# Performance work log

Measured on AMD Instinct MI355X. Metric: run time of the kernel, lower is better.

Reference implementation:

```python
import jax, jax.numpy as jnp
import numpy as np

N_EMBD = 1024
N_HEADS = 16
HEAD_DIM = N_EMBD // N_HEADS


def setup_inputs() -> dict:
    key = jax.random.key(0)
    ks = jax.random.split(key, 6)
    s = 1.0 / np.sqrt(N_EMBD)
    x = jax.random.normal(ks[0], (2, 2048, N_EMBD), dtype=jnp.float32)
    # torch Linear weights are [out, in]; y = x @ W.T
    Wk = jax.random.uniform(ks[1], (N_EMBD, N_EMBD), jnp.float32, -s, s)
    Wq = jax.random.uniform(ks[2], (N_EMBD, N_EMBD), jnp.float32, -s, s)
    Wv = jax.random.uniform(ks[3], (N_EMBD, N_EMBD), jnp.float32, -s, s)
    Wp = jax.random.uniform(ks[4], (N_EMBD, N_EMBD), jnp.float32, -s, s)
    bp = jax.random.uniform(ks[5], (N_EMBD,), jnp.float32, -s, s)
    return {"x": x, "Wq": Wq, "Wk": Wk, "Wv": Wv, "Wp": Wp, "bp": bp}


def reference(x, Wq, Wk, Wv, Wp, bp):
    B, T, C = x.shape
    H, D = N_HEADS, HEAD_DIM
    # projections (torch Linear: x @ W.T), reshape to [B, H, T, D]
    q = (x @ Wq.T).reshape(B, T, H, D).transpose(0, 2, 1, 3)
    k = (x @ Wk.T).reshape(B, T, H, D).transpose(0, 2, 1, 3)
    v = (x @ Wv.T).reshape(B, T, H, D).transpose(0, 2, 1, 3)
    # scaled causal attention, full [B,H,T,T] scores (faithful to original)
    att = jnp.einsum('bhqd,bhkd->bhqk', q, k) * (D ** -0.5)
    causal = jnp.tril(jnp.ones((T, T), dtype=bool))
    att = jnp.where(causal[None, None], att, -jnp.inf)
    att = jax.nn.softmax(att, axis=-1)
    out = jnp.einsum('bhqk,bhkd->bhqd', att, v)
    out = out.transpose(0, 2, 1, 3).reshape(B, T, C)
    return out @ Wp.T + bp
```

## Files before the change

kernel.cpp:

```cpp
#include <hip/hip_runtime.h>

typedef __bf16 bf16;
typedef __bf16 bf16x8 __attribute__((ext_vector_type(8)));
typedef float f32x4 __attribute__((ext_vector_type(4)));

typedef __attribute__((address_space(1))) const void as1_void;
typedef __attribute__((address_space(3))) void as3_void;

#define DEV __device__ __forceinline__
#define NEG_BIG (-1.0e30f)


DEV void async_load16(const void* g, void* l) {
  __builtin_amdgcn_global_load_lds((as1_void*)g, (as3_void*)l, 16, 0, 0);
}
DEV bf16x8 load8(const bf16* p) { bf16x8 v; __builtin_memcpy(&v, p, 16); return v; }
DEV void store8(bf16* p, bf16x8 v) { __builtin_memcpy(p, &v, 16); }

DEV int sniff_bf16(const unsigned short* __restrict__ xr) {
  const int lane = threadIdx.x & 63;
  const unsigned short w = xr[lane * 2];
  const int e = (w >> 7) & 0xFF;
  const bool sane = ((w & 0x7FFF) == 0) || (e >= 97 && e <= 157);
  return __popcll(__ballot(sane)) >= 48;
}

struct ConvArgs {
  const void* src[6];
  bf16* dst[6];
  int n[6];
};

__global__ __launch_bounds__(256) void convert_kernel(ConvArgs a) {
  const int isbf = sniff_bf16((const unsigned short*)a.src[0]);
  const int t = blockIdx.y;
  const int n = a.n[t];
  bf16* d = a.dst[t];
  const int stride = gridDim.x * 256 * 8;
  if (isbf) {
    const bf16* s = (const bf16*)a.src[t];
    for (int i = (blockIdx.x * 256 + threadIdx.x) * 8; i < n; i += stride)
      store8(d + i, load8(s + i));
  } else {
    const float* s = (const float*)a.src[t];
    for (int i = (blockIdx.x * 256 + threadIdx.x) * 8; i < n; i += stride) {
      float tmp[8];
      __builtin_memcpy(tmp, s + i, 32);
      bf16x8 v;
#pragma unroll
      for (int j = 0; j < 8; ++j) v[j] = (bf16)tmp[j];
      store8(d + i, v);
    }
  }
}

DEV void gemm_core_128(const bf16* A, const bf16* W, int K, int m0, int n0,
                       f32x4 (&acc)[4][4]) {
  __shared__ alignas(16) bf16 As[2][128 * 64];
  __shared__ alignas(16) bf16 Bs[2][128 * 64];
  const int tid = threadIdx.x;
  const int lane = tid & 63;
  const int wid = tid >> 6;
  const int wm = (wid >> 1) << 6;
  const int wn = (wid & 1) << 6;
  const int lr = lane & 15;
  const int lg = lane >> 4;

  const f32x4 zero = {0.f, 0.f, 0.f, 0.f};
#pragma unroll
  for (int i = 0; i < 4; ++i)
#pragma unroll
    for (int j = 0; j < 4; ++j) acc[i][j] = zero;

  const int nt = K >> 6;

  auto stage = [&](int buf, int t) {
    const int k0 = t << 6;
#pragma unroll
    for (int it = 0; it < 4; ++it) {
      const int lin = it * 256 + tid;
      const int row = lin >> 3;
      const int sc = (lin & 7) ^ (row & 7);
      async_load16(A + (size_t)(m0 + row) * K + (size_t)(k0 + sc * 8),
                   &As[buf][0] + lin * 8);
      async_load16(W + (size_t)(n0 + row) * K + (size_t)(k0 + sc * 8),
                   &Bs[buf][0] + lin * 8);
    }
  };

  auto compute = [&](int buf) {
    const bf16* as = &As[buf][0];
    const bf16* bs = &Bs[buf][0];
#pragma unroll
    for (int kk = 0; kk < 64; kk += 32) {
      const int g0 = kk >> 3;
      bf16x8 af[4], bfr[4];
#pragma unroll
      for (int i = 0; i < 4; ++i) {
        const int r = wm + i * 16 + lr;
        af[i] = load8(as + ((r << 3) | ((g0 + lg) ^ (r & 7))) * 8);
      }
#pragma unroll
      for (int j = 0; j < 4; ++j) {
        const int r = wn + j * 16 + lr;
        bfr[j] = load8(bs + ((r << 3) | ((g0 + lg) ^ (r & 7))) * 8);
      }
#pragma unroll
      for (int i = 0; i < 4; ++i)
#pragma unroll
        for (int j = 0; j < 4; ++j)
          acc[i][j] = __builtin_amdgcn_mfma_f32_16x16x32_bf16(af[i], bfr[j], acc[i][j], 0, 0, 0);
    }
  };

  stage(0, 0);
  stage(1, 1);
  int cur = 0;
  for (int t = 0; t < nt; ++t) {
    if (t + 1 < nt) asm volatile("s_waitcnt vmcnt(8)" ::: "memory");
    else            asm volatile("s_waitcnt vmcnt(0)" ::: "memory");
    __builtin_amdgcn_s_barrier();
    compute(cur);
    asm volatile("s_waitcnt lgkmcnt(0)" ::: "memory");
    __builtin_amdgcn_s_barrier();
    if (t + 2 < nt) stage(cur, t + 2);
    cur ^= 1;
  }
}

DEV size_t frag_idx(int row, int col) {
  return ((size_t)(((col >> 5) * 4 + ((row >> 4) & 3)) * 64 + ((col >> 3) & 3) * 16 + (row & 15)) << 3)
         | (size_t)(col & 7);
}

__global__ __launch_bounds__(256) void qkv_proj_kernel(
    const bf16* __restrict__ x, const bf16* __restrict__ Wq,
    const bf16* __restrict__ Wk, const bf16* __restrict__ Wv,
    bf16* __restrict__ q_ws, bf16* __restrict__ k_ws, bf16* __restrict__ vt_ws) {
  const int L = blockIdx.x;
  const int xcd = L & 7;
  const int i2 = L >> 3;
  const int m0 = (xcd * 4 + (i2 & 3)) << 7;
  const int rest = i2 >> 2;
  const int n0 = (rest & 7) << 7;
  const int mode = rest >> 3;
  const bf16* W = (mode == 0) ? Wq : (mode == 1) ? Wk : Wv;
  f32x4 acc[4][4];
  gemm_core_128(x, W, 1024, m0, n0, acc);

  const int tid = threadIdx.x;
  const int lane = tid & 63, wid = tid >> 6;
  const int wm = (wid >> 1) << 6, wn = (wid & 1) << 6;
  const int lr = lane & 15, lg = lane >> 4;
  bf16* out = (mode == 0) ? q_ws : (mode == 1) ? k_ws : vt_ws;
#pragma unroll
  for (int i = 0; i < 4; ++i) {
#pragma unroll
    for (int r = 0; r < 4; ++r) {
      const int m = m0 + wm + i * 16 + lg * 4 + r;
      const int b = m >> 11, t = m & 2047;
#pragma unroll
      for (int j = 0; j < 4; ++j) {
        const int n = n0 + wn + j * 16 + lr;
        const int h = n >> 6, d = n & 63;
        const float v = acc[i][j][r];
        const size_t base = ((size_t)(b * 16 + h) << 17) + ((size_t)(t >> 6) << 12);
        const size_t idx = base + ((mode < 2) ? frag_idx(t & 63, d) : frag_idx(d, t & 63));
        out[idx] = (bf16)v;
      }
    }
  }
}

__global__ __launch_bounds__(256, 2) void attn_kernel(
    const bf16* __restrict__ q_ws, const bf16* __restrict__ k_ws,
    const bf16* __restrict__ vt_ws, bf16* __restrict__ a_ws) {
  const int L = blockIdx.x;
  const int xcd = L & 7;
  const int bh = xcd * 4 + ((L >> 3) & 3);
  const int pr = L >> 5;
  const int tid = threadIdx.x;
  const int lane = tid & 63, w = tid >> 6;
  const int lr = lane & 15, lg = lane >> 4;
  const int fo = lg * 16 + lr;

  __shared__ alignas(16) bf16 Ps[4][16 * 72];
  bf16* ps = &Ps[w][0];

  const size_t hb = (size_t)bh << 17;
  const int b = bh >> 4, h = bh & 15;
  const f32x4 zero = {0.f, 0.f, 0.f, 0.f};

  for (int ph = 0; ph < 2; ++ph) {
    const int qt = ph ? (31 - pr) : pr;
    const size_t qtb = hb + ((size_t)qt << 12);

    bf16x8 aq[2];
#pragma unroll
    for (int c2 = 0; c2 < 2; ++c2)
      aq[c2] = load8(q_ws + qtb + (size_t)(((c2 * 4 + w) * 64 + fo) << 3));

    f32x4 o_acc[4];
#pragma unroll
    for (int j = 0; j < 4; ++j) o_acc[j] = zero;
    float lsum[4] = {0.f, 0.f, 0.f, 0.f};

    auto load_k = [&](bf16x8 (&bk)[4][2], int kt) {
      const size_t ktb = hb + ((size_t)kt << 12);
#pragma unroll
      for (int j = 0; j < 4; ++j)
#pragma unroll
        for (int c2 = 0; c2 < 2; ++c2)
          bk[j][c2] = load8(k_ws + ktb + (size_t)(((c2 * 4 + j) * 64 + fo) << 3));
    };

    auto step = [&](const bf16x8 (&bk)[4][2], int kt, bool diag) {
      const size_t ktb = hb + ((size_t)kt << 12);
      bf16x8 bv[4][2];
#pragma unroll
      for (int j = 0; j < 4; ++j)
#pragma unroll
        for (int c2 = 0; c2 < 2; ++c2)
          bv[j][c2] = load8(vt_ws + ktb + (size_t)(((c2 * 4 + j) * 64 + fo) << 3));

      f32x4 s[4];
#pragma unroll
      for (int j = 0; j < 4; ++j) {
        s[j] = __builtin_amdgcn_mfma_f32_16x16x32_bf16(aq[0], bk[j][0], zero, 0, 0, 0);
        s[j] = __builtin_amdgcn_mfma_f32_16x16x32_bf16(aq[1], bk[j][1], s[j], 0, 0, 0);
      }
      float p[4][4];
#pragma unroll
      for (int j = 0; j < 4; ++j) {
#pragma unroll
        for (int r = 0; r < 4; ++r) {
          float v = s[j][r] * 0.125f;
          if (diag && (j * 16 + lr) > (w * 16 + lg * 4 + r)) v = NEG_BIG;
          p[j][r] = __expf(v);
        }
      }
#pragma unroll
      for (int r = 0; r < 4; ++r)
        lsum[r] += (p[0][r] + p[1][r]) + (p[2][r] + p[3][r]);
#pragma unroll
      for (int j = 0; j < 4; ++j)
#pragma unroll
        for (int r = 0; r < 4; ++r)
          ps[(lg * 4 + r) * 72 + j * 16 + lr] = (bf16)p[j][r];
#pragma unroll
      for (int c2 = 0; c2 < 2; ++c2) {
        const bf16x8 ap = load8(ps + lr * 72 + c2 * 32 + lg * 8);
#pragma unroll
        for (int j = 0; j < 4; ++j)
          o_acc[j] = __builtin_amdgcn_mfma_f32_16x16x32_bf16(ap, bv[j][c2], o_acc[j], 0, 0, 0);
      }
    };

    bf16x8 bkA[4][2], bkB[4][2];
    const int n = qt;
    load_k(bkA, qt);
    if (n > 0) load_k(bkB, 0);
    step(bkA, qt, true);
    int kt = 0;
    while (kt + 1 < n) {
      load_k(bkA, kt + 1);
      step(bkB, kt, false);
      if (kt + 2 < n) load_k(bkB, kt + 2);
      step(bkA, kt + 1, false);
      kt += 2;
    }
    if (kt < n) step(bkB, kt, false);

    float l_i[4];
#pragma unroll
    for (int r = 0; r < 4; ++r) {
      float v = lsum[r];
#pragma unroll
      for (int off = 1; off < 16; off <<= 1) v += __shfl_xor(v, off, 64);
      l_i[r] = v;
    }

#pragma unroll
    for (int r = 0; r < 4; ++r) {
      const int t = qt * 64 + w * 16 + lg * 4 + r;
      const float inv = 1.f / l_i[r];
#pragma unroll
      for (int j = 0; j < 4; ++j) {
        const size_t idx = (((size_t)(b * 2048 + t)) << 10) | (size_t)(h * 64 + j * 16 + lr);
        a_ws[idx] = (bf16)(o_acc[j][r] * inv);
      }
    }
  }
}

__global__ __launch_bounds__(256) void out_proj_kernel(
    const bf16* __restrict__ A, const bf16* __restrict__ Wp,
    const bf16* __restrict__ bp, void* __restrict__ out,
    const unsigned short* __restrict__ xraw) {
  const int L = blockIdx.x;
  const int xcd = L & 7;
  const int i2 = L >> 3;
  const int m0 = (xcd * 4 + (i2 & 3)) << 7;
  const int n0 = (i2 >> 2) << 7;
  f32x4 acc[4][4];
  gemm_core_128(A, Wp, 1024, m0, n0, acc);

  const int tid = threadIdx.x;
  const int lane = tid & 63, wid = tid >> 6;
  const int wm = (wid >> 1) << 6, wn = (wid & 1) << 6;
  const int lr = lane & 15, lg = lane >> 4;
  const int isbf = sniff_bf16(xraw);
#pragma unroll
  for (int i = 0; i < 4; ++i) {
#pragma unroll
    for (int r = 0; r < 4; ++r) {
      const int m = m0 + wm + i * 16 + lg * 4 + r;
#pragma unroll
      for (int j = 0; j < 4; ++j) {
        const int n = n0 + wn + j * 16 + lr;
        const float v = acc[i][j][r] + (float)bp[n];
        const size_t idx = ((size_t)m << 10) | (size_t)n;
        if (isbf) ((bf16*)out)[idx] = (bf16)v;
        else      ((float*)out)[idx] = v;
      }
    }
  }
}

extern "C" void kernel_launch(void* const* d_in, const int* in_sizes, int n_in,
                              void* d_out, int out_size, void* d_ws, size_t ws_size,
                              hipStream_t stream) {
  (void)in_sizes; (void)n_in; (void)out_size;
  if (ws_size < (50u << 20)) return;

  char* ws = (char*)d_ws;
  bf16* q_ws  = (bf16*)(ws);
  bf16* k_ws  = (bf16*)(ws + (8u << 20));
  bf16* vt_ws = (bf16*)(ws + (16u << 20));
  bf16* a_ws  = (bf16*)(ws + (24u << 20));
  bf16* xc    = (bf16*)(ws + (32u << 20));
  bf16* Wqc   = (bf16*)(ws + (40u << 20));
  bf16* Wkc   = (bf16*)(ws + (42u << 20));
  bf16* Wvc   = (bf16*)(ws + (44u << 20));
  bf16* Wpc   = (bf16*)(ws + (46u << 20));
  bf16* bpc   = (bf16*)(ws + (48u << 20));

  ConvArgs ca;
  ca.src[0] = d_in[0]; ca.dst[0] = xc;  ca.n[0] = 4096 * 1024;
  ca.src[1] = d_in[1]; ca.dst[1] = Wqc; ca.n[1] = 1024 * 1024;
  ca.src[2] = d_in[2]; ca.dst[2] = Wkc; ca.n[2] = 1024 * 1024;
  ca.src[3] = d_in[3]; ca.dst[3] = Wvc; ca.n[3] = 1024 * 1024;
  ca.src[4] = d_in[4]; ca.dst[4] = Wpc; ca.n[4] = 1024 * 1024;
  ca.src[5] = d_in[5]; ca.dst[5] = bpc; ca.n[5] = 1024;
  convert_kernel<<<dim3(512, 6), 256, 0, stream>>>(ca);

  qkv_proj_kernel<<<768, 256, 0, stream>>>(xc, Wqc, Wkc, Wvc, q_ws, k_ws, vt_ws);
  attn_kernel<<<512, 256, 0, stream>>>(q_ws, k_ws, vt_ws, a_ws);
  out_proj_kernel<<<256, 256, 0, stream>>>(a_ws, Wpc, bpc, d_out,
                                           (const unsigned short*)d_in[0]);
}
```

Measured before the change: 182.2 us.

## Use triple-buffered K=32 pipelined GEMM core for QKV projection

Adds a GEMM core that stages 128x32 tiles of A and W into three LDS buffers via async global-to-LDS loads with an XOR swizzle, issuing loads two steps ahead and waiting with a single barrier per K step. The QKV projection kernel now uses it instead of the double-buffered K=64 core. The aim is to hide global load latency and cut barrier stalls, at the cost of more loop iterations and smaller compute per stage.

Result: faster. 178.3 us (-2.1%).

```diff
diff --git a/kernel.cpp b/kernel.cpp
--- a/kernel.cpp
+++ b/kernel.cpp
@@ -54,6 +54,92 @@
   }
 }
 
+DEV void gemm_core_128_p(const bf16* A, const bf16* W, const int K, int m0, int n0,
+                         f32x4 (&acc)[4][4]) {
+  __shared__ alignas(16) bf16 As[3][128 * 32];
+  __shared__ alignas(16) bf16 Bs[3][128 * 32];
+  const int tid = threadIdx.x;
+  const int lane = tid & 63;
+  const int wid = tid >> 6;
+  const int wm = (wid >> 1) << 6;
+  const int wn = (wid & 1) << 6;
+  const int lr = lane & 15;
+  const int lg = lane >> 4;
+
+  size_t srcA[2], srcB[2];
+  int ldsoff[2];
+#pragma unroll
+  for (int it = 0; it < 2; ++it) {
+    const int lin = it * 256 + tid;
+    const int lr2 = lin >> 3, c = lin & 7;
+    const int u = c ^ (lr2 & 7);
+    const int r = lr2 * 2 + (u >> 2);
+    const int g = u & 3;
+    srcA[it] = (size_t)(m0 + r) * K + (size_t)(g * 8);
+    srcB[it] = (size_t)(n0 + r) * K + (size_t)(g * 8);
+    ldsoff[it] = lin * 8;
+  }
+  int offA[4], offB[4];
+#pragma unroll
+  for (int i = 0; i < 4; ++i) {
+    const int r = wm + i * 16 + lr;
+    const int cc = (lg | ((r & 1) << 2)) ^ ((r >> 1) & 7);
+    offA[i] = (((r >> 1) << 3) | cc) * 8;
+  }
+#pragma unroll
+  for (int j = 0; j < 4; ++j) {
+    const int r = wn + j * 16 + lr;
+    const int cc = (lg | ((r & 1) << 2)) ^ ((r >> 1) & 7);
+    offB[j] = (((r >> 1) << 3) | cc) * 8;
+  }
+
+  const f32x4 zero = {0.f, 0.f, 0.f, 0.f};
+#pragma unroll
+  for (int i = 0; i < 4; ++i)
+#pragma unroll
+    for (int j = 0; j < 4; ++j) acc[i][j] = zero;
+
+  const int nt = K >> 5;
+
+  auto stage = [&](int buf, int t) {
+    const size_t k0 = (size_t)(t << 5);
+#pragma unroll
+    for (int it = 0; it < 2; ++it) {
+      async_load16(A + srcA[it] + k0, &As[buf][0] + ldsoff[it]);
+      async_load16(W + srcB[it] + k0, &Bs[buf][0] + ldsoff[it]);
+    }
+  };
+
+  auto compute = [&](int buf) {
+    const bf16* as = &As[buf][0];
+    const bf16* bs = &Bs[buf][0];
+    bf16x8 af[4], bfr[4];
+#pragma unroll
+    for (int i = 0; i < 4; ++i) af[i] = load8(as + offA[i]);
+#pragma unroll
+    for (int j = 0; j < 4; ++j) bfr[j] = load8(bs + offB[j]);
+    __builtin_amdgcn_s_setprio(1);
+#pragma unroll
+    for (int i = 0; i < 4; ++i)
+#pragma unroll
+      for (int j = 0; j < 4; ++j)
+        acc[i][j] = __builtin_amdgcn_mfma_f32_16x16x32_bf16(af[i], bfr[j], acc[i][j], 0, 0, 0);
+    __builtin_amdgcn_s_setprio(0);
+  };
+
+  stage(0, 0);
+  stage(1, 1);
+  int b0 = 0, b1 = 1, b2 = 2;
+  for (int t = 0; t < nt; ++t) {
+    if (t + 1 < nt) asm volatile("s_waitcnt vmcnt(4)" ::: "memory");
+    else            asm volatile("s_waitcnt vmcnt(0)" ::: "memory");
+    __builtin_amdgcn_s_barrier();
+    if (t + 2 < nt) stage(b2, t + 2);
+    compute(b0);
+    const int tmp = b0; b0 = b1; b1 = b2; b2 = tmp;
+  }
+}
+
 DEV void gemm_core_128(const bf16* A, const bf16* W, int K, int m0, int n0,
                        f32x4 (&acc)[4][4]) {
   __shared__ alignas(16) bf16 As[2][128 * 64];
@@ -146,7 +232,7 @@
   const int mode = rest >> 3;
   const bf16* W = (mode == 0) ? Wq : (mode == 1) ? Wk : Wv;
   f32x4 acc[4][4];
-  gemm_core_128(x, W, 1024, m0, n0, acc);
+  gemm_core_128_p(x, W, 1024, m0, n0, acc);
 
   const int tid = threadIdx.x;
   const int lane = tid & 63, wid = tid >> 6;
```

## Triple-buffer GEMM with K=32 tiles and one-tile-per-block attention grid

Applied to the files above, without the earlier changes.

The shared GEMM core moves from double-buffered 64-wide K tiles to triple-buffered 32-wide K tiles. Source and LDS offsets are precomputed once, one barrier per iteration is removed by issuing the next stage before compute, and MFMA issue priority is raised with setprio. The attention kernel now gives each block a single query tile, heaviest first, on a 1024-block grid instead of pairing light and heavy tiles in 512 blocks. This trades explicit load balancing for more parallelism and dynamic scheduling, and the GEMM uses smaller tiles with deeper prefetch.

New measurement: 183.5 us. No clear change (+0.8%).

```diff
diff --git a/kernel.cpp b/kernel.cpp
--- a/kernel.cpp
+++ b/kernel.cpp
@@ -54,10 +54,10 @@
   }
 }
 
-DEV void gemm_core_128(const bf16* A, const bf16* W, int K, int m0, int n0,
-                       f32x4 (&acc)[4][4]) {
-  __shared__ alignas(16) bf16 As[2][128 * 64];
-  __shared__ alignas(16) bf16 Bs[2][128 * 64];
+DEV void gemm_core_128_p(const bf16* A, const bf16* W, const int K, int m0, int n0,
+                         f32x4 (&acc)[4][4]) {
+  __shared__ alignas(16) bf16 As[3][128 * 32];
+  __shared__ alignas(16) bf16 Bs[3][128 * 32];
   const int tid = threadIdx.x;
   const int lane = tid & 63;
   const int wid = tid >> 6;
@@ -66,65 +66,77 @@
   const int lr = lane & 15;
   const int lg = lane >> 4;
 
+  size_t srcA[2], srcB[2];
+  int ldsoff[2];
+#pragma unroll
+  for (int it = 0; it < 2; ++it) {
+    const int lin = it * 256 + tid;
+    const int lr2 = lin >> 3, c = lin & 7;
+    const int u = c ^ (lr2 & 7);
+    const int r = lr2 * 2 + (u >> 2);
+    const int g = u & 3;
+    srcA[it] = (size_t)(m0 + r) * K + (size_t)(g * 8);
+    srcB[it] = (size_t)(n0 + r) * K + (size_t)(g * 8);
+    ldsoff[it] = lin * 8;
+  }
+  int offA[4], offB[4];
+#pragma unroll
+  for (int i = 0; i < 4; ++i) {
+    const int r = wm + i * 16 + lr;
+    const int cc = (lg | ((r & 1) << 2)) ^ ((r >> 1) & 7);
+    offA[i] = (((r >> 1) << 3) | cc) * 8;
+  }
+#pragma unroll
+  for (int j = 0; j < 4; ++j) {
+    const int r = wn + j * 16 + lr;
+    const int cc = (lg | ((r & 1) << 2)) ^ ((r >> 1) & 7);
+    offB[j] = (((r >> 1) << 3) | cc) * 8;
+  }
+
   const f32x4 zero = {0.f, 0.f, 0.f, 0.f};
 #pragma unroll
   for (int i = 0; i < 4; ++i)
 #pragma unroll
     for (int j = 0; j < 4; ++j) acc[i][j] = zero;
 
-  const int nt = K >> 6;
+  const int nt = K >> 5;
 
   auto stage = [&](int buf, int t) {
-    const int k0 = t << 6;
-#pragma unroll
-    for (int it = 0; it < 4; ++it) {
-      const int lin = it * 256 + tid;
-      const int row = lin >> 3;
-      const int sc = (lin & 7) ^ (row & 7);
-      async_load16(A + (size_t)(m0 + row) * K + (size_t)(k0 + sc * 8),
-                   &As[buf][0] + lin * 8);
-      async_load16(W + (size_t)(n0 + row) * K + (size_t)(k0 + sc * 8),
-                   &Bs[buf][0] + lin * 8);
+    const size_t k0 = (size_t)(t << 5);
+#pragma unroll
+    for (int it = 0; it < 2; ++it) {
+      async_load16(A + srcA[it] + k0, &As[buf][0] + ldsoff[it]);
+      async_load16(W + srcB[it] + k0, &Bs[buf][0] + ldsoff[it]);
     }
   };
 
   auto compute = [&](int buf) {
     const bf16* as = &As[buf][0];
     const bf16* bs = &Bs[buf][0];
-#pragma unroll
-    for (int kk = 0; kk < 64; kk += 32) {
-      const int g0 = kk >> 3;
-      bf16x8 af[4], bfr[4];
-#pragma unroll
-      for (int i = 0; i < 4; ++i) {
-        const int r = wm + i * 16 + lr;
-        af[i] = load8(as + ((r << 3) | ((g0 + lg) ^ (r & 7))) * 8);
-      }
-#pragma unroll
-      for (int j = 0; j < 4; ++j) {
-        const int r = wn + j * 16 + lr;
-        bfr[j] = load8(bs + ((r << 3) | ((g0 + lg) ^ (r & 7))) * 8);
-      }
-#pragma unroll
-      for (int i = 0; i < 4; ++i)
-#pragma unroll
-        for (int j = 0; j < 4; ++j)
-          acc[i][j] = __builtin_amdgcn_mfma_f32_16x16x32_bf16(af[i], bfr[j], acc[i][j], 0, 0, 0);
-    }
+    bf16x8 af[4], bfr[4];
+#pragma unroll
+    for (int i = 0; i < 4; ++i) af[i] = load8(as + offA[i]);
+#pragma unroll
+    for (int j = 0; j < 4; ++j) bfr[j] = load8(bs + offB[j]);
+    __builtin_amdgcn_s_setprio(1);
+#pragma unroll
+    for (int i = 0; i < 4; ++i)
+#pragma unroll
+      for (int j = 0; j < 4; ++j)
+        acc[i][j] = __builtin_amdgcn_mfma_f32_16x16x32_bf16(af[i], bfr[j], acc[i][j], 0, 0, 0);
+    __builtin_amdgcn_s_setprio(0);
   };
 
   stage(0, 0);
   stage(1, 1);
-  int cur = 0;
+  int b0 = 0, b1 = 1, b2 = 2;
   for (int t = 0; t < nt; ++t) {
-    if (t + 1 < nt) asm volatile("s_waitcnt vmcnt(8)" ::: "memory");
+    if (t + 1 < nt) asm volatile("s_waitcnt vmcnt(4)" ::: "memory");
     else            asm volatile("s_waitcnt vmcnt(0)" ::: "memory");
     __builtin_amdgcn_s_barrier();
-    compute(cur);
-    asm volatile("s_waitcnt lgkmcnt(0)" ::: "memory");
-    __builtin_amdgcn_s_barrier();
-    if (t + 2 < nt) stage(cur, t + 2);
-    cur ^= 1;
+    if (t + 2 < nt) stage(b2, t + 2);
+    compute(b0);
+    const int tmp = b0; b0 = b1; b1 = b2; b2 = tmp;
   }
 }
 
@@ -146,7 +158,7 @@
   const int mode = rest >> 3;
   const bf16* W = (mode == 0) ? Wq : (mode == 1) ? Wk : Wv;
   f32x4 acc[4][4];
-  gemm_core_128(x, W, 1024, m0, n0, acc);
+  gemm_core_128_p(x, W, 1024, m0, n0, acc);
 
   const int tid = threadIdx.x;
   const int lane = tid & 63, wid = tid >> 6;
@@ -178,7 +190,7 @@
   const int L = blockIdx.x;
   const int xcd = L & 7;
   const int bh = xcd * 4 + ((L >> 3) & 3);
-  const int pr = L >> 5;
+  const int qt = 31 - (L >> 5);
   const int tid = threadIdx.x;
   const int lane = tid & 63, w = tid >> 6;
   const int lr = lane & 15, lg = lane >> 4;
@@ -191,104 +203,101 @@
   const int b = bh >> 4, h = bh & 15;
   const f32x4 zero = {0.f, 0.f, 0.f, 0.f};
 
-  for (int ph = 0; ph < 2; ++ph) {
-    const int qt = ph ? (31 - pr) : pr;
-    const size_t qtb = hb + ((size_t)qt << 12);
-
-    bf16x8 aq[2];
-#pragma unroll
-    for (int c2 = 0; c2 < 2; ++c2)
-      aq[c2] = load8(q_ws + qtb + (size_t)(((c2 * 4 + w) * 64 + fo) << 3));
-
-    f32x4 o_acc[4];
-#pragma unroll
-    for (int j = 0; j < 4; ++j) o_acc[j] = zero;
-    float lsum[4] = {0.f, 0.f, 0.f, 0.f};
-
-    auto load_k = [&](bf16x8 (&bk)[4][2], int kt) {
-      const size_t ktb = hb + ((size_t)kt << 12);
+  const size_t qtb = hb + ((size_t)qt << 12);
+
+  bf16x8 aq[2];
+#pragma unroll
+  for (int c2 = 0; c2 < 2; ++c2)
+    aq[c2] = load8(q_ws + qtb + (size_t)(((c2 * 4 + w) * 64 + fo) << 3));
+
+  f32x4 o_acc[4];
+#pragma unroll
+  for (int j = 0; j < 4; ++j) o_acc[j] = zero;
+  float lsum[4] = {0.f, 0.f, 0.f, 0.f};
+
+  auto load_k = [&](bf16x8 (&bk)[4][2], int kt) {
+    const size_t ktb = hb + ((size_t)kt << 12);
+#pragma unroll
+    for (int j = 0; j < 4; ++j)
+#pragma unroll
+      for (int c2 = 0; c2 < 2; ++c2)
+        bk[j][c2] = load8(k_ws + ktb + (size_t)(((c2 * 4 + j) * 64 + fo) << 3));
+  };
+
+  auto step = [&](const bf16x8 (&bk)[4][2], int kt, bool diag) {
+    const size_t ktb = hb + ((size_t)kt << 12);
+    bf16x8 bv[4][2];
+#pragma unroll
+    for (int j = 0; j < 4; ++j)
+#pragma unroll
+      for (int c2 = 0; c2 < 2; ++c2)
+        bv[j][c2] = load8(vt_ws + ktb + (size_t)(((c2 * 4 + j) * 64 + fo) << 3));
+
+    f32x4 s[4];
+#pragma unroll
+    for (int j = 0; j < 4; ++j) {
+      s[j] = __builtin_amdgcn_mfma_f32_16x16x32_bf16(aq[0], bk[j][0], zero, 0, 0, 0);
+      s[j] = __builtin_amdgcn_mfma_f32_16x16x32_bf16(aq[1], bk[j][1], s[j], 0, 0, 0);
+    }
+    float p[4][4];
+#pragma unroll
+    for (int j = 0; j < 4; ++j) {
+#pragma unroll
+      for (int r = 0; r < 4; ++r) {
+        float v = s[j][r] * 0.125f;
+        if (diag && (j * 16 + lr) > (w * 16 + lg * 4 + r)) v = NEG_BIG;
+        p[j][r] = __expf(v);
+      }
+    }
+#pragma unroll
+    for (int r = 0; r < 4; ++r)
+      lsum[r] += (p[0][r] + p[1][r]) + (p[2][r] + p[3][r]);
+#pragma unroll
+    for (int j = 0; j < 4; ++j)
+#pragma unroll
+      for (int r = 0; r < 4; ++r)
+        ps[(lg * 4 + r) * 72 + j * 16 + lr] = (bf16)p[j][r];
+#pragma unroll
+    for (int c2 = 0; c2 < 2; ++c2) {
+      const bf16x8 ap = load8(ps + lr * 72 + c2 * 32 + lg * 8);
 #pragma unroll
       for (int j = 0; j < 4; ++j)
-#pragma unroll
-        for (int c2 = 0; c2 < 2; ++c2)
-          bk[j][c2] = load8(k_ws + ktb + (size_t)(((c2 * 4 + j) * 64 + fo) << 3));
-    };
-
-    auto step = [&](const bf16x8 (&bk)[4][2], int kt, bool diag) {
-      const size_t ktb = hb + ((size_t)kt << 12);
-      bf16x8 bv[4][2];
-#pragma unroll
-      for (int j = 0; j < 4; ++j)
-#pragma unroll
-        for (int c2 = 0; c2 < 2; ++c2)
-          bv[j][c2] = load8(vt_ws + ktb + (size_t)(((c2 * 4 + j) * 64 + fo) << 3));
-
-      f32x4 s[4];
-#pragma unroll
-      for (int j = 0; j < 4; ++j) {
-        s[j] = __builtin_amdgcn_mfma_f32_16x16x32_bf16(aq[0], bk[j][0], zero, 0, 0, 0);
-        s[j] = __builtin_amdgcn_mfma_f32_16x16x32_bf16(aq[1], bk[j][1], s[j], 0, 0, 0);
-      }
-      float p[4][4];
-#pragma unroll
-      for (int j = 0; j < 4; ++j) {
-#pragma unroll
-        for (int r = 0; r < 4; ++r) {
-          float v = s[j][r] * 0.125f;
-          if (diag && (j * 16 + lr) > (w * 16 + lg * 4 + r)) v = NEG_BIG;
-          p[j][r] = __expf(v);
-        }
-      }
-#pragma unroll
-      for (int r = 0; r < 4; ++r)
-        lsum[r] += (p[0][r] + p[1][r]) + (p[2][r] + p[3][r]);
-#pragma unroll
-      for (int j = 0; j < 4; ++j)
-#pragma unroll
-        for (int r = 0; r < 4; ++r)
-          ps[(lg * 4 + r) * 72 + j * 16 + lr] = (bf16)p[j][r];
-#pragma unroll
-      for (int c2 = 0; c2 < 2; ++c2) {
-        const bf16x8 ap = load8(ps + lr * 72 + c2 * 32 + lg * 8);
-#pragma unroll
-        for (int j = 0; j < 4; ++j)
-          o_acc[j] = __builtin_amdgcn_mfma_f32_16x16x32_bf16(ap, bv[j][c2], o_acc[j], 0, 0, 0);
-      }
-    };
-
-    bf16x8 bkA[4][2], bkB[4][2];
-    const int n = qt;
-    load_k(bkA, qt);
-    if (n > 0) load_k(bkB, 0);
-    step(bkA, qt, true);
-    int kt = 0;
-    while (kt + 1 < n) {
-      load_k(bkA, kt + 1);
-      step(bkB, kt, false);
-      if (kt + 2 < n) load_k(bkB, kt + 2);
-      step(bkA, kt + 1, false);
-      kt += 2;
-    }
-    if (kt < n) step(bkB, kt, false);
-
-    float l_i[4];
-#pragma unroll
-    for (int r = 0; r < 4; ++r) {
-      float v = lsum[r];
-#pragma unroll
-      for (int off = 1; off < 16; off <<= 1) v += __shfl_xor(v, off, 64);
-      l_i[r] = v;
-    }
-
-#pragma unroll
-    for (int r = 0; r < 4; ++r) {
-      const int t = qt * 64 + w * 16 + lg * 4 + r;
-      const float inv = 1.f / l_i[r];
-#pragma unroll
-      for (int j = 0; j < 4; ++j) {
-        const size_t idx = (((size_t)(b * 2048 + t)) << 10) | (size_t)(h * 64 + j * 16 + lr);
-        a_ws[idx] = (bf16)(o_acc[j][r] * inv);
-      }
+        o_acc[j] = __builtin_amdgcn_mfma_f32_16x16x32_bf16(ap, bv[j][c2], o_acc[j], 0, 0, 0);
+    }
+  };
+
+  bf16x8 bkA[4][2], bkB[4][2];
+  const int n = qt;
+  load_k(bkA, qt);
+  if (n > 0) load_k(bkB, 0);
+  step(bkA, qt, true);
+  int kt = 0;
+  while (kt + 1 < n) {
+    load_k(bkA, kt + 1);
+    step(bkB, kt, false);
+    if (kt + 2 < n) load_k(bkB, kt + 2);
+    step(bkA, kt + 1, false);
+    kt += 2;
+  }
+  if (kt < n) step(bkB, kt, false);
+
+  float l_i[4];
+#pragma unroll
+  for (int r = 0; r < 4; ++r) {
+    float v = lsum[r];
+#pragma unroll
+    for (int off = 1; off < 16; off <<= 1) v += __shfl_xor(v, off, 64);
+    l_i[r] = v;
+  }
+
+#pragma unroll
+  for (int r = 0; r < 4; ++r) {
+    const int t = qt * 64 + w * 16 + lg * 4 + r;
+    const float inv = 1.f / l_i[r];
+#pragma unroll
+    for (int j = 0; j < 4; ++j) {
+      const size_t idx = (((size_t)(b * 2048 + t)) << 10) | (size_t)(h * 64 + j * 16 + lr);
+      a_ws[idx] = (bf16)(o_acc[j][r] * inv);
     }
   }
 }
@@ -303,7 +312,7 @@
   const int m0 = (xcd * 4 + (i2 & 3)) << 7;
   const int n0 = (i2 >> 2) << 7;
   f32x4 acc[4][4];
-  gemm_core_128(A, Wp, 1024, m0, n0, acc);
+  gemm_core_128_p(A, Wp, 1024, m0, n0, acc);
 
   const int tid = threadIdx.x;
   const int lane = tid & 63, wid = tid >> 6;
@@ -355,7 +364,7 @@
   convert_kernel<<<dim3(512, 6), 256, 0, stream>>>(ca);
 
   qkv_proj_kernel<<<768, 256, 0, stream>>>(xc, Wqc, Wkc, Wvc, q_ws, k_ws, vt_ws);
-  attn_kernel<<<512, 256, 0, stream>>>(q_ws, k_ws, vt_ws, a_ws);
+  attn_kernel<<<1024, 256, 0, stream>>>(q_ws, k_ws, vt_ws, a_ws);
   out_proj_kernel<<<256, 256, 0, stream>>>(a_ws, Wpc, bpc, d_out,
                                            (const unsigned short*)d_in[0]);
 }
```
